# Performance work log

Hardware: AMD Instinct MI355X
Metric: run time of the kernel (lower is better)

## Reference

```python
import jax, jax.numpy as jnp
import numpy as np

D_MODEL = 1024
N_HEADS = 16
D_HEAD = D_MODEL // N_HEADS
B, S = 4, 2048


def setup_inputs() -> dict:
    key = jax.random.key(0)
    ks = jax.random.split(key, 9)
    s = 1.0 / np.sqrt(D_MODEL)
    inp = {
        "x": jax.random.normal(ks[0], (B, S, D_MODEL), dtype=jnp.float32),
        "W_q": jax.random.uniform(ks[1], (D_MODEL, D_MODEL), jnp.float32, -s, s),
        "b_q": jax.random.uniform(ks[2], (D_MODEL,), jnp.float32, -s, s),
        "W_k": jax.random.uniform(ks[3], (D_MODEL, D_MODEL), jnp.float32, -s, s),
        "b_k": jax.random.uniform(ks[4], (D_MODEL,), jnp.float32, -s, s),
        "W_v": jax.random.uniform(ks[5], (D_MODEL, D_MODEL), jnp.float32, -s, s),
        "b_v": jax.random.uniform(ks[6], (D_MODEL,), jnp.float32, -s, s),
        "W_o": jax.random.uniform(ks[7], (D_MODEL, D_MODEL), jnp.float32, -s, s),
        "b_o": jax.random.uniform(ks[8], (D_MODEL,), jnp.float32, -s, s),
    }
    return inp


def reference(x, W_q, b_q, W_k, b_k, W_v, b_v, W_o, b_o):
    b, s, d = x.shape
    # Project and split heads: [b, h, s, d_head]
    def split(t):
        return t.reshape(b, s, N_HEADS, D_HEAD).transpose(0, 2, 1, 3)
    Q = split(x @ W_q + b_q)
    K = split(x @ W_k + b_k)
    V = split(x @ W_v + b_v)
    scores = jnp.einsum('bhqd,bhkd->bhqk', Q, K) / np.sqrt(D_HEAD).astype(np.float32)
    causal = jnp.triu(jnp.full((s, s), -jnp.inf, dtype=scores.dtype), k=1)
    scores = scores + causal
    attn = jax.nn.softmax(scores, axis=-1)  # dropout p=0 -> identity
    ctx = jnp.einsum('bhqk,bhkd->bhqd', attn, V)
    ctx = ctx.transpose(0, 2, 1, 3).reshape(b, s, d)
    return ctx @ W_o + b_o
```

## Files before the change

kernel.cpp:

```cpp
#include <hip/hip_runtime.h>
#include <stdint.h>

#define B_    4
#define S_    2048
#define DM    1024
#define NH    16
#define DH    64
#define BH    (B_ * NH)
#define MROWS (B_ * S_)
#define LOG2E 1.4426950408889634f

typedef __attribute__((ext_vector_type(8))) short short8;
typedef __attribute__((ext_vector_type(4))) float f32x4;
typedef __attribute__((ext_vector_type(16))) float f32x16;
typedef __attribute__((ext_vector_type(4))) unsigned int u32x4;

__device__ __forceinline__ unsigned short f2bf(float f) {
  unsigned int u = __float_as_uint(f);
  u = (u + 0x7FFFu + ((u >> 16) & 1u)) >> 16;
  return (unsigned short)u;
}
__device__ __forceinline__ unsigned int pack_bf16(float lo, float hi) {
  unsigned int a = (__float_as_uint(lo) + 0x8000u) >> 16;
  unsigned int b = (__float_as_uint(hi) + 0x8000u) & 0xFFFF0000u;
  return a | b;
}

__device__ __forceinline__ void gll16(const void* g, const void* l) {
  __builtin_amdgcn_global_load_lds(
      (__attribute__((address_space(1))) void*)(unsigned long long)g,
      (__attribute__((address_space(3))) void*)(unsigned int)(unsigned long long)l,
      16, 0, 0);
}

__global__ __launch_bounds__(256) void prep_kernel(
    const float* __restrict__ x,
    const float* __restrict__ Wq, const float* __restrict__ Wk,
    const float* __restrict__ Wv, const float* __restrict__ Wo,
    unsigned short* __restrict__ xb,
    unsigned short* __restrict__ wt_qkv, unsigned short* __restrict__ wt_o) {
  __shared__ float t[32][33];
  const int z = blockIdx.z;
  if (z >= 4) {
    size_t lb = (size_t)(z - 4) * 1024 + blockIdx.y * 32 + blockIdx.x;
    size_t i = (lb * 256 + threadIdx.x) * 8;
    float4 a = *(const float4*)(x + i);
    float4 b = *(const float4*)(x + i + 4);
    short8 o;
    o[0] = (short)f2bf(a.x); o[1] = (short)f2bf(a.y);
    o[2] = (short)f2bf(a.z); o[3] = (short)f2bf(a.w);
    o[4] = (short)f2bf(b.x); o[5] = (short)f2bf(b.y);
    o[6] = (short)f2bf(b.z); o[7] = (short)f2bf(b.w);
    *(short8*)(xb + i) = o;
    return;
  }
  const float* W = z == 0 ? Wq : z == 1 ? Wk : z == 2 ? Wv : Wo;
  unsigned short* dst = z < 3 ? wt_qkv + (size_t)z * DM * DM : wt_o;
  const int nb = blockIdx.x * 32, kb = blockIdx.y * 32;
  const int tx = threadIdx.x & 31, ty = threadIdx.x >> 5;
#pragma unroll
  for (int p = 0; p < 4; ++p) {
    int r = ty + p * 8;
    t[r][tx] = W[(size_t)(kb + r) * DM + nb + tx];
  }
  __syncthreads();
#pragma unroll
  for (int p = 0; p < 4; ++p) {
    int r = ty + p * 8;
    dst[(size_t)(nb + r) * DM + kb + tx] = f2bf(t[tx][r]);
  }
}

__global__ __launch_bounds__(256) void transpose_v_kernel(
    const unsigned short* __restrict__ V, unsigned short* __restrict__ Vt) {
  __shared__ unsigned short t[32][33];
  const int bh = blockIdx.z;
  const int sb = blockIdx.x * 32, db = blockIdx.y * 32;
  const int tx = threadIdx.x & 31, ty = threadIdx.x >> 5;
  const unsigned short* Vp = V + (size_t)bh * S_ * DH;
  unsigned short* Vtp = Vt + (size_t)bh * DH * S_;
#pragma unroll
  for (int p = 0; p < 4; ++p) {
    int r = ty + p * 8;
    t[r][tx] = Vp[(size_t)(sb + r) * DH + db + tx];
  }
  __syncthreads();
#pragma unroll
  for (int p = 0; p < 4; ++p) {
    int r = ty + p * 8;
    Vtp[(size_t)(db + r) * S_ + sb + tx] = t[tx][r];
  }
}

__device__ __forceinline__ void gemm_core(const unsigned short* __restrict__ A,
                                          const unsigned short* __restrict__ Bt,
                                          int m0, int n0,
                                          unsigned short* As, unsigned short* Bs,
                                          f32x16 (&acc)[2][2]) {
  const int tid = threadIdx.x;
  const int lane = tid & 63, wave = tid >> 6;
  const int l31 = lane & 31, half = lane >> 5;
  const int wm = (wave >> 1) * 64, wn = (wave & 1) * 64;

  for (int kk = 0; kk < DM; kk += 64) {
#pragma unroll
    for (int p = 0; p < 4; ++p) {
      int idx = p * 256 + tid;
      int row = idx >> 3, ch = idx & 7;
      int sc = (ch ^ (row & 7)) << 3;
      gll16(A  + (size_t)(m0 + row) * DM + kk + sc, As + idx * 8);
      gll16(Bt + (size_t)(n0 + row) * DM + kk + sc, Bs + idx * 8);
    }
    __syncthreads();
#pragma unroll
    for (int ks = 0; ks < 4; ++ks) {
      short8 af[2], bf[2];
#pragma unroll
      for (int mi = 0; mi < 2; ++mi) {
        int row = wm + mi * 32 + l31;
        af[mi] = *(const short8*)&As[row * 64 + (((ks * 2 + half) ^ (l31 & 7)) << 3)];
      }
#pragma unroll
      for (int nj = 0; nj < 2; ++nj) {
        int row = wn + nj * 32 + l31;
        bf[nj] = *(const short8*)&Bs[row * 64 + (((ks * 2 + half) ^ (l31 & 7)) << 3)];
      }
#pragma unroll
      for (int mi = 0; mi < 2; ++mi)
#pragma unroll
        for (int nj = 0; nj < 2; ++nj)
          acc[mi][nj] = __builtin_amdgcn_mfma_f32_32x32x16_bf16(af[mi], bf[nj], acc[mi][nj], 0, 0, 0);
    }
    __syncthreads();
  }
}

__global__ __launch_bounds__(256) void gemm_qkv_kernel(
    const unsigned short* __restrict__ xb, const unsigned short* __restrict__ wt,
    const float* __restrict__ bq, const float* __restrict__ bk, const float* __restrict__ bv,
    unsigned short* __restrict__ Qb, unsigned short* __restrict__ Kb,
    unsigned short* __restrict__ Vb) {
  __shared__ unsigned short As[128 * 64];
  __shared__ unsigned short Bs[128 * 64];
  f32x16 acc[2][2] = {};
  const int m0 = blockIdx.y * 128, n0 = blockIdx.x * 128;
  gemm_core(xb, wt, m0, n0, As, Bs, acc);

  const int tid = threadIdx.x, lane = tid & 63, wave = tid >> 6;
  const int l31 = lane & 31, half = lane >> 5;
  const int wm = (wave >> 1) * 64, wn = (wave & 1) * 64;
  const int which = n0 >> 10;
  const float* bias = which == 0 ? bq : (which == 1 ? bk : bv);
  unsigned short* dst = which == 0 ? Qb : (which == 1 ? Kb : Vb);
  const float scale = (which == 0) ? 0.125f * LOG2E : 1.0f;
  const int nb = n0 - (which << 10);
#pragma unroll
  for (int nj = 0; nj < 2; ++nj) {
    int n10 = nb + wn + nj * 32 + l31;
    float bsv = bias[n10];
    int h = n10 >> 6, d = n10 & 63;
#pragma unroll
    for (int mi = 0; mi < 2; ++mi) {
#pragma unroll
      for (int reg = 0; reg < 16; ++reg) {
        int m = m0 + wm + mi * 32 + (reg & 3) + 8 * (reg >> 2) + 4 * half;
        int b = m >> 11, s = m & 2047;
        float v = (acc[mi][nj][reg] + bsv) * scale;
        dst[(((size_t)(b * NH + h)) * S_ + s) * DH + d] = f2bf(v);
      }
    }
  }
}

__global__ __launch_bounds__(256) void gemm_out_kernel(
    const unsigned short* __restrict__ ctx, const unsigned short* __restrict__ wto,
    const float* __restrict__ bo, float* __restrict__ out) {
  __shared__ unsigned short As[128 * 64];
  __shared__ unsigned short Bs[128 * 64];
  f32x16 acc[2][2] = {};
  const int m0 = blockIdx.y * 128, n0 = blockIdx.x * 128;
  gemm_core(ctx, wto, m0, n0, As, Bs, acc);

  const int tid = threadIdx.x, lane = tid & 63, wave = tid >> 6;
  const int l31 = lane & 31, half = lane >> 5;
  const int wm = (wave >> 1) * 64, wn = (wave & 1) * 64;
#pragma unroll
  for (int nj = 0; nj < 2; ++nj) {
    int n = n0 + wn + nj * 32 + l31;
    float bsv = bo[n];
#pragma unroll
    for (int mi = 0; mi < 2; ++mi) {
#pragma unroll
      for (int reg = 0; reg < 16; ++reg) {
        int m = m0 + wm + mi * 32 + (reg & 3) + 8 * (reg >> 2) + 4 * half;
        out[(size_t)m * DM + n] = acc[mi][nj][reg] + bsv;
      }
    }
  }
}

__global__ __launch_bounds__(256, 3) void attn_kernel(
    const unsigned short* __restrict__ Qb, const unsigned short* __restrict__ Kb,
    const unsigned short* __restrict__ Vt, unsigned short* __restrict__ ctx) {
  __shared__ unsigned short Ks[2][128 * 64];
  __shared__ unsigned short Vs[64 * 128];

  const int tid = threadIdx.x, lane = tid & 63, wave = tid >> 6;
  const int col = lane & 15, quad = lane >> 4;
  const int bh = blockIdx.x;
  const int qt = 15 - blockIdx.y;
  const int b = bh >> 4, h = bh & 15;

  const unsigned short* Qp = Qb + ((size_t)bh * S_ + qt * 128) * DH;
  const unsigned short* Kbase = Kb + (size_t)bh * S_ * DH;
  const unsigned short* Vbase = Vt + (size_t)bh * DH * S_;

#pragma unroll
  for (int p = 0; p < 4; ++p) {
    int idx = p * 256 + tid;
    int row = idx >> 3, ch = idx & 7;
    int sc = (ch ^ (row & 7)) << 3;
    gll16(Kbase + row * 64 + sc, &Ks[0][0] + idx * 8);
  }
  short8 qf[2][2];
#pragma unroll
  for (int i = 0; i < 2; ++i)
#pragma unroll
    for (int ksd = 0; ksd < 2; ++ksd)
      qf[i][ksd] = *(const short8*)(Qp + (wave * 32 + i * 16 + col) * 64 + ksd * 32 + quad * 8);
  __syncthreads();

  f32x4 o[2][4] = {};
  f32x4 lacc[2] = {};

  const int idxA = (col + ((lane & 16) << 1)) << 2;
  const int idxB = idxA + 64;
  const bool hij = (lane & 32) != 0;

  for (int kt = 0; kt <= qt; ++kt) {
    const int cur = kt & 1;
    const unsigned short* Vp = Vbase + kt * 128;
#pragma unroll
    for (int p = 0; p < 4; ++p) {
      int idx = p * 256 + tid;
      int row = idx >> 4, ch = idx & 15;
      int sc = (ch & 8) | ((ch ^ row) & 7);
      gll16(Vp + (size_t)row * S_ + sc * 8, Vs + idx * 8);
    }
    if (kt < qt) {
      const unsigned short* Kp = Kbase + (size_t)(kt + 1) * 128 * DH;
#pragma unroll
      for (int p = 0; p < 4; ++p) {
        int idx = p * 256 + tid;
        int row = idx >> 3, ch = idx & 7;
        int sc = (ch ^ (row & 7)) << 3;
        gll16(Kp + row * 64 + sc, &Ks[cur ^ 1][0] + idx * 8);
      }
    }

    f32x4 sa[2][8];
#pragma unroll
    for (int jt = 0; jt < 8; ++jt) {
      int row = jt * 16 + col;
      short8 kf0 = *(const short8*)&Ks[cur][row * 64 + ((quad ^ (row & 7)) << 3)];
      short8 kf1 = *(const short8*)&Ks[cur][row * 64 + (((4 + quad) ^ (row & 7)) << 3)];
#pragma unroll
      for (int i = 0; i < 2; ++i) {
        f32x4 c = {-8.f, -8.f, -8.f, -8.f};
        c = __builtin_amdgcn_mfma_f32_16x16x32_bf16(kf0, qf[i][0], c, 0, 0, 0);
        c = __builtin_amdgcn_mfma_f32_16x16x32_bf16(kf1, qf[i][1], c, 0, 0, 0);
        sa[i][jt] = c;
      }
    }

    if (kt == qt) {
#pragma unroll
      for (int i = 0; i < 2; ++i) {
        int ql = wave * 32 + i * 16 + col;
#pragma unroll
        for (int jt = 0; jt < 8; ++jt)
#pragma unroll
          for (int r = 0; r < 4; ++r)
            if (jt * 16 + quad * 4 + r > ql) sa[i][jt][r] = -__builtin_inff();
      }
    }

    unsigned int ppk[2][8][2];
#pragma unroll
    for (int i = 0; i < 2; ++i)
#pragma unroll
      for (int jt = 0; jt < 8; ++jt) {
        f32x4 p;
#pragma unroll
        for (int c4 = 0; c4 < 4; ++c4) {
          p[c4] = __builtin_amdgcn_exp2f(sa[i][jt][c4]);
          lacc[i][c4] += p[c4];
        }
        ppk[i][jt][0] = pack_bf16(p[0], p[1]);
        ppk[i][jt][1] = pack_bf16(p[2], p[3]);
      }

    __syncthreads();

#pragma unroll
    for (int ks = 0; ks < 4; ++ks) {
      short8 vf[4];
#pragma unroll
      for (int jo = 0; jo < 4; ++jo) {
        int row = jo * 16 + col;
        int c = ks * 4 + quad;
        int ch = (c & 8) | ((c ^ row) & 7);
        vf[jo] = *(const short8*)&Vs[row * 128 + ch * 8];
      }
#pragma unroll
      for (int i = 0; i < 2; ++i) {
        int p0 = (int)ppk[i][2 * ks][0], p1 = (int)ppk[i][2 * ks][1];
        int q0 = (int)ppk[i][2 * ks + 1][0], q1 = (int)ppk[i][2 * ks + 1][1];
        int a0 = __builtin_amdgcn_ds_bpermute(idxA, p0);
        int b0 = __builtin_amdgcn_ds_bpermute(idxA, q0);
        int a1 = __builtin_amdgcn_ds_bpermute(idxA, p1);
        int b1 = __builtin_amdgcn_ds_bpermute(idxA, q1);
        int a2 = __builtin_amdgcn_ds_bpermute(idxB, p0);
        int b2 = __builtin_amdgcn_ds_bpermute(idxB, q0);
        int a3 = __builtin_amdgcn_ds_bpermute(idxB, p1);
        int b3 = __builtin_amdgcn_ds_bpermute(idxB, q1);
        u32x4 uu;
        uu[0] = (unsigned)(hij ? b0 : a0);
        uu[1] = (unsigned)(hij ? b1 : a1);
        uu[2] = (unsigned)(hij ? b2 : a2);
        uu[3] = (unsigned)(hij ? b3 : a3);
        short8 af = __builtin_bit_cast(short8, uu);
#pragma unroll
        for (int jo = 0; jo < 4; ++jo)
          o[i][jo] = __builtin_amdgcn_mfma_f32_16x16x32_bf16(af, vf[jo], o[i][jo], 0, 0, 0);
      }
    }
    __syncthreads();
  }

#pragma unroll
  for (int i = 0; i < 2; ++i) {
    float l = (lacc[i][0] + lacc[i][1]) + (lacc[i][2] + lacc[i][3]);
    l += __shfl_xor(l, 16);
    l += __shfl_xor(l, 32);
#pragma unroll
    for (int r = 0; r < 4; ++r) {
      float lr = __shfl(l, ((lane >> 4) << 2) + r);
      float inv = __builtin_amdgcn_rcpf(lr);
      int s = qt * 128 + wave * 32 + i * 16 + quad * 4 + r;
#pragma unroll
      for (int jo = 0; jo < 4; ++jo) {
        int d = jo * 16 + col;
        ctx[((size_t)(b * S_ + s)) * DM + h * DH + d] = f2bf(o[i][jo][r] * inv);
      }
    }
  }
}

extern "C" void kernel_launch(void* const* d_in, const int* in_sizes, int n_in,
                              void* d_out, int out_size, void* d_ws, size_t ws_size,
                              hipStream_t stream) {
  (void)in_sizes; (void)n_in; (void)out_size; (void)ws_size;
  const float* x  = (const float*)d_in[0];
  const float* Wq = (const float*)d_in[1];
  const float* bq = (const float*)d_in[2];
  const float* Wk = (const float*)d_in[3];
  const float* bk = (const float*)d_in[4];
  const float* Wv = (const float*)d_in[5];
  const float* bv = (const float*)d_in[6];
  const float* Wo = (const float*)d_in[7];
  const float* bo = (const float*)d_in[8];
  float* out = (float*)d_out;

  char* ws = (char*)d_ws;
  size_t off = 0;
  auto carve = [&](size_t bytes) -> char* {
    char* p = ws + off;
    off += (bytes + 255) & ~(size_t)255;
    return p;
  };
  unsigned short* xb  = (unsigned short*)carve((size_t)MROWS * DM * 2);
  unsigned short* wtq = (unsigned short*)carve((size_t)3 * DM * DM * 2);
  unsigned short* wto = (unsigned short*)carve((size_t)DM * DM * 2);
  unsigned short* Qb  = (unsigned short*)carve((size_t)BH * S_ * DH * 2);
  unsigned short* Kb  = (unsigned short*)carve((size_t)BH * S_ * DH * 2);
  unsigned short* Vb  = (unsigned short*)carve((size_t)BH * S_ * DH * 2);
  unsigned short* Vt  = (unsigned short*)carve((size_t)BH * S_ * DH * 2);
  unsigned short* ctx = Vb;

  prep_kernel<<<dim3(32, 32, 8), 256, 0, stream>>>(x, Wq, Wk, Wv, Wo, xb, wtq, wto);
  gemm_qkv_kernel<<<dim3(24, 64), 256, 0, stream>>>(xb, wtq, bq, bk, bv, Qb, Kb, Vb);
  transpose_v_kernel<<<dim3(64, 2, 64), 256, 0, stream>>>(Vb, Vt);
  attn_kernel<<<dim3(64, 16), 256, 0, stream>>>(Qb, Kb, Vt, ctx);
  gemm_out_kernel<<<dim3(8, 64), 256, 0, stream>>>(ctx, wto, bo, out);
}
```

Measured before the change: 269.7 us.

## Single-buffer K/V tiles in attention to raise occupancy, add GEMM launch bounds

The attention kernel drops the double-buffered K tile and loads both K and V for the next tile after the PV stage, halving K LDS and raising the occupancy hint from 3 to 5 blocks. The GEMM kernels get a minimum-blocks-per-SM hint of 4. This cuts LDS footprint to allow more resident workgroups, which hides latency through occupancy. In exchange, loads of the next tile no longer overlap the current tile's QK compute within a block, and the tighter register cap may cause spills.

```diff
diff --git a/kernel.cpp b/kernel.cpp
--- a/kernel.cpp
+++ b/kernel.cpp
@@ -135,7 +135,7 @@
   }
 }
 
-__global__ __launch_bounds__(256) void gemm_qkv_kernel(
+__global__ __launch_bounds__(256, 4) void gemm_qkv_kernel(
     const unsigned short* __restrict__ xb, const unsigned short* __restrict__ wt,
     const float* __restrict__ bq, const float* __restrict__ bk, const float* __restrict__ bv,
     unsigned short* __restrict__ Qb, unsigned short* __restrict__ Kb,
@@ -172,7 +172,7 @@
   }
 }
 
-__global__ __launch_bounds__(256) void gemm_out_kernel(
+__global__ __launch_bounds__(256, 4) void gemm_out_kernel(
     const unsigned short* __restrict__ ctx, const unsigned short* __restrict__ wto,
     const float* __restrict__ bo, float* __restrict__ out) {
   __shared__ unsigned short As[128 * 64];
@@ -199,10 +199,10 @@
   }
 }
 
-__global__ __launch_bounds__(256, 3) void attn_kernel(
+__global__ __launch_bounds__(256, 5) void attn_kernel(
     const unsigned short* __restrict__ Qb, const unsigned short* __restrict__ Kb,
     const unsigned short* __restrict__ Vt, unsigned short* __restrict__ ctx) {
-  __shared__ unsigned short Ks[2][128 * 64];
+  __shared__ unsigned short Ks[128 * 64];
   __shared__ unsigned short Vs[64 * 128];
 
   const int tid = threadIdx.x, lane = tid & 63, wave = tid >> 6;
@@ -218,9 +218,16 @@
 #pragma unroll
   for (int p = 0; p < 4; ++p) {
     int idx = p * 256 + tid;
-    int row = idx >> 3, ch = idx & 7;
-    int sc = (ch ^ (row & 7)) << 3;
-    gll16(Kbase + row * 64 + sc, &Ks[0][0] + idx * 8);
+    {
+      int row = idx >> 3, ch = idx & 7;
+      int sc = (ch ^ (row & 7)) << 3;
+      gll16(Kbase + row * 64 + sc, Ks + idx * 8);
+    }
+    {
+      int row = idx >> 4, ch = idx & 15;
+      int sc = (ch & 8) | ((ch ^ row) & 7);
+      gll16(Vbase + (size_t)row * S_ + sc * 8, Vs + idx * 8);
+    }
   }
   short8 qf[2][2];
 #pragma unroll
@@ -228,7 +235,6 @@
 #pragma unroll
     for (int ksd = 0; ksd < 2; ++ksd)
       qf[i][ksd] = *(const short8*)(Qp + (wave * 32 + i * 16 + col) * 64 + ksd * 32 + quad * 8);
-  __syncthreads();
 
   f32x4 o[2][4] = {};
   f32x4 lacc[2] = {};
@@ -238,32 +244,14 @@
   const bool hij = (lane & 32) != 0;
 
   for (int kt = 0; kt <= qt; ++kt) {
-    const int cur = kt & 1;
-    const unsigned short* Vp = Vbase + kt * 128;
-#pragma unroll
-    for (int p = 0; p < 4; ++p) {
-      int idx = p * 256 + tid;
-      int row = idx >> 4, ch = idx & 15;
-      int sc = (ch & 8) | ((ch ^ row) & 7);
-      gll16(Vp + (size_t)row * S_ + sc * 8, Vs + idx * 8);
-    }
-    if (kt < qt) {
-      const unsigned short* Kp = Kbase + (size_t)(kt + 1) * 128 * DH;
-#pragma unroll
-      for (int p = 0; p < 4; ++p) {
-        int idx = p * 256 + tid;
-        int row = idx >> 3, ch = idx & 7;
-        int sc = (ch ^ (row & 7)) << 3;
-        gll16(Kp + row * 64 + sc, &Ks[cur ^ 1][0] + idx * 8);
-      }
-    }
+    __syncthreads();
 
     f32x4 sa[2][8];
 #pragma unroll
     for (int jt = 0; jt < 8; ++jt) {
       int row = jt * 16 + col;
-      short8 kf0 = *(const short8*)&Ks[cur][row * 64 + ((quad ^ (row & 7)) << 3)];
-      short8 kf1 = *(const short8*)&Ks[cur][row * 64 + (((4 + quad) ^ (row & 7)) << 3)];
+      short8 kf0 = *(const short8*)&Ks[row * 64 + ((quad ^ (row & 7)) << 3)];
+      short8 kf1 = *(const short8*)&Ks[row * 64 + (((4 + quad) ^ (row & 7)) << 3)];
 #pragma unroll
       for (int i = 0; i < 2; ++i) {
         f32x4 c = {-8.f, -8.f, -8.f, -8.f};
@@ -299,8 +287,6 @@
         ppk[i][jt][0] = pack_bf16(p[0], p[1]);
         ppk[i][jt][1] = pack_bf16(p[2], p[3]);
       }
-
-    __syncthreads();
 
 #pragma unroll
     for (int ks = 0; ks < 4; ++ks) {
@@ -335,7 +321,27 @@
           o[i][jo] = __builtin_amdgcn_mfma_f32_16x16x32_bf16(af, vf[jo], o[i][jo], 0, 0, 0);
       }
     }
+
     __syncthreads();
+
+    if (kt < qt) {
+      const unsigned short* Kp = Kbase + (size_t)(kt + 1) * 128 * DH;
+      const unsigned short* Vp = Vbase + (kt + 1) * 128;
+#pragma unroll
+      for (int p = 0; p < 4; ++p) {
+        int idx = p * 256 + tid;
+        {
+          int row = idx >> 3, ch = idx & 7;
+          int sc = (ch ^ (row & 7)) << 3;
+          gll16(Kp + row * 64 + sc, Ks + idx * 8);
+        }
+        {
+          int row = idx >> 4, ch = idx & 15;
+          int sc = (ch & 8) | ((ch ^ row) & 7);
+          gll16(Vp + (size_t)row * S_ + sc * 8, Vs + idx * 8);
+        }
+      }
+    }
   }
 
 #pragma unroll
```

Result: slower. 600.6 us (+122.7%).
